# Kernel tuning notes

Hardware: AMD Instinct MI355X
Metric: run time of the kernel (lower is better)

The kernel has to match this reference:

```python
import jax, jax.numpy as jnp
import numpy as np

B, N, O, K, F = 4, 256, 5, 5, 256
H, D, DFF = 4, 64, 1024  # num_heads, KQ_len, FFN hidden
EPS = 1e-5


def setup_inputs() -> dict:
    key = jax.random.key(0)
    ks = jax.random.split(key, 16)
    s = 0.05
    p = lambda k, shape: (jax.random.normal(k, shape, jnp.float32) * s)
    return {
        "x": jax.random.normal(ks[0], (B, N, O, K, K, F), jnp.float32),
        "Wq": p(ks[1], (H * D, F)), "bq": p(ks[2], (H * D,)),
        "Wk": p(ks[3], (H * D, F)), "bk": p(ks[4], (H * D,)),
        "Wv": p(ks[5], (H * D, F)), "bv": p(ks[6], (H * D,)),
        "Wf": p(ks[7], (F, F)), "bf": p(ks[8], (F,)),
        "ln1_w": jnp.ones((N, O, F), jnp.float32), "ln1_b": jnp.zeros((N, O, F), jnp.float32),
        "ln2_w": jnp.ones((N, O, F), jnp.float32), "ln2_b": jnp.zeros((N, O, F), jnp.float32),
        "W1": p(ks[9], (DFF, F)), "b1": p(ks[10], (DFF,)),
        "W2": p(ks[11], (F, DFF)), "b2": p(ks[12], (F,)),
    }


def _layer_norm3(x, w, b):
    # torch LayerNorm with normalized_shape=[N, O, F]: stats over last 3 dims
    mu = jnp.mean(x, axis=(1, 2, 3), keepdims=True)
    var = jnp.var(x, axis=(1, 2, 3), keepdims=True)
    return (x - mu) * jax.lax.rsqrt(var + EPS) * w + b


def _split_heads(y):
    # [B,N,O,K,K,H*D] -> [B,N,O,H,K,K,D]
    return y.reshape(B, N, O, K, K, H, D).transpose(0, 1, 2, 5, 3, 4, 6)


def reference(x, Wq, bq, Wk, bk, Wv, bv, Wf, bf,
              ln1_w, ln1_b, ln2_w, ln2_b, W1, b1, W2, b2):
    q = _split_heads(x @ Wq.T + bq)
    k = _split_heads(x @ Wk.T + bk)
    v = _split_heads(x @ Wv.T + bv)
    c = K // 2
    qc = q[:, :, :, :, c, c, :]  # center query [B,N,O,H,D]
    # tile+mul+sum == dot of center query against every patch key
    scores = jnp.einsum('bnohd,bnohijd->bnohij', qc, k) / np.sqrt(float(D))
    w = jax.nn.softmax(scores.reshape(B, N, O, H, K * K), axis=-1)
    merged = jnp.einsum('bnohp,bnohpd->bnohd', w, v.reshape(B, N, O, H, K * K, D))
    merged = merged.reshape(B, N, O, H * D)
    attent = merged @ Wf.T + bf  # dropout = identity (eval)
    out1 = _layer_norm3(attent, ln1_w, ln1_b)
    ffn = jax.nn.relu(out1 @ W1.T + b1) @ W2.T + b2
    return _layer_norm3(out1 + ffn, ln2_w, ln2_b)
```

## Files before the change

kernel.cpp:

```cpp
#include <hip/hip_runtime.h>
#include <hip/hip_bf16.h>

#define FF 256
#define HH 4
#define DD 64
#define PP 25
#define SITES 5120
#define SPB 1280
#define DFF 1024
#define LN_ELEMS 327680

typedef const __hip_bfloat16* bfp;
typedef __hip_bfloat16* bfw;
typedef __attribute__((ext_vector_type(8))) short bf16x8;
typedef __attribute__((ext_vector_type(4))) float f32x4;

__device__ __forceinline__ float b2f(const __hip_bfloat16 v) { return __bfloat162float(v); }
__device__ __forceinline__ bool detect_bf(const unsigned* dt) {
    return dt[0] == 0x3F803F80u;
}
__device__ __forceinline__ float ldin(const void* p, size_t i, bool bf) {
    return bf ? __bfloat162float(((const __hip_bfloat16*)p)[i]) : ((const float*)p)[i];
}
__device__ __forceinline__ unsigned short f2bu(float f) {
    __hip_bfloat16 h = __float2bfloat16(f);
    return *(unsigned short*)&h;
}
__device__ __forceinline__ uint4 ldin8(const void* p, size_t i, bool bf) {
    if (bf) return *(const uint4*)((const unsigned short*)p + i);
    const float* f = (const float*)p + i;
    const float4 a = *(const float4*)f;
    const float4 b = *(const float4*)(f + 4);
    unsigned short u[8] = { f2bu(a.x), f2bu(a.y), f2bu(a.z), f2bu(a.w),
                            f2bu(b.x), f2bu(b.y), f2bu(b.z), f2bu(b.w) };
    return *(uint4*)u;
}

template<int RELU, int RES, int GATHER, int STATS, int BINT>
__global__ __launch_bounds__(256) void gemm_mfma(
    const void* xg, bfp Ab, int lda,
    const void* Bm, int ldb, const void* bias,
    bfp resid, int ldr, bfw C, int ldc, int Kc,
    int aoh, size_t boh, int bioh, int coh,
    float* __restrict__ red, const unsigned* dt)
{
    const bool bf = detect_bf(dt);
    const int h = blockIdx.z;
    Ab += (size_t)h * aoh;
    const size_t boff = (size_t)h * boh;
    const size_t biasoff = (size_t)h * bioh;
    C += (size_t)h * coh;

    __shared__ unsigned short Als[64][72];
    __shared__ unsigned short Bls[64][72];
    __shared__ float rs4[4], rss4[4];
    const int tid = threadIdx.x;
    const int lane = tid & 63;
    const int w = tid >> 6;
    const int m0 = blockIdx.y * 64;
    const int n0 = blockIdx.x * 64;
    const int r8 = tid >> 3;
    const int c8 = (tid & 7) * 8;

    f32x4 acc[4];
    #pragma unroll
    for (int mi = 0; mi < 4; ++mi) acc[mi] = (f32x4){0.f, 0.f, 0.f, 0.f};

    for (int k0 = 0; k0 < Kc; k0 += 64) {
        #pragma unroll
        for (int rr = 0; rr < 2; ++rr) {
            const int row = r8 + rr * 32;
            uint4 v;
            if (GATHER) v = ldin8(xg, ((size_t)(m0 + row) * PP + 12) * FF + (k0 + c8), bf);
            else        v = *(const uint4*)(Ab + (size_t)(m0 + row) * lda + (k0 + c8));
            *(uint4*)&Als[row][c8] = v;
        }
        #pragma unroll
        for (int rr = 0; rr < 2; ++rr) {
            const int row = r8 + rr * 32;
            const size_t bi = boff + (size_t)(n0 + row) * ldb + (k0 + c8);
            uint4 v;
            if (BINT) v = *(const uint4*)((const unsigned short*)Bm + bi);
            else      v = ldin8(Bm, bi, bf);
            *(uint4*)&Bls[row][c8] = v;
        }
        __syncthreads();
        #pragma unroll
        for (int ks = 0; ks < 2; ++ks) {
            const int kq = ks * 32 + (lane >> 4) * 8;
            const bf16x8 bfr = *(const bf16x8*)&Bls[w * 16 + (lane & 15)][kq];
            #pragma unroll
            for (int mi = 0; mi < 4; ++mi) {
                const bf16x8 afr = *(const bf16x8*)&Als[mi * 16 + (lane & 15)][kq];
                acc[mi] = __builtin_amdgcn_mfma_f32_16x16x32_bf16(afr, bfr, acc[mi], 0, 0, 0);
            }
        }
        __syncthreads();
    }

    const int col = n0 + w * 16 + (lane & 15);
    const int quad = lane >> 4;
    const float bvv = bias ? ldin(bias, biasoff + col, bf) : 0.f;
    float s_ = 0.f, ss_ = 0.f;
    #pragma unroll
    for (int mi = 0; mi < 4; ++mi) {
        #pragma unroll
        for (int r = 0; r < 4; ++r) {
            const int row = m0 + mi * 16 + quad * 4 + r;
            float v = acc[mi][r] + bvv;
            if (RES)  v += b2f(resid[(size_t)row * ldr + col]);
            if (RELU) v = fmaxf(v, 0.0f);
            if (STATS) { s_ += v; ss_ += v * v; }
            C[(size_t)row * ldc + col] = __float2bfloat16(v);
        }
    }
    if (STATS) {
        #pragma unroll
        for (int o = 32; o > 0; o >>= 1) { s_ += __shfl_down(s_, o); ss_ += __shfl_down(ss_, o); }
        if (lane == 0) { rs4[w] = s_; rss4[w] = ss_; }
        __syncthreads();
        if (tid == 0) {
            const int batch = m0 / SPB;
            atomicAdd(&red[batch * 2 + 0], rs4[0] + rs4[1] + rs4[2] + rs4[3]);
            atomicAdd(&red[batch * 2 + 1], rss4[0] + rss4[1] + rss4[2] + rss4[3]);
        }
    }
}

__global__ __launch_bounds__(256) void wkT_k(const void* Wk, bfw WkT, const unsigned* dt)
{
    const bool bf = detect_bf(dt);
    const int idx = blockIdx.x * 256 + threadIdx.x;
    const int d = idx & 63;
    const int f = (idx >> 6) & 255;
    const int h = idx >> 14;
    WkT[idx] = __float2bfloat16(ldin(Wk, (size_t)(h * DD + d) * FF + f, bf));
}

__global__ __launch_bounds__(256) void attn_site(const void* x, bfp qk, bfw xw,
                                                 const unsigned* dt)
{
    __shared__ unsigned short xsb[32][264];
    __shared__ unsigned short qkb[HH][FF];
    __shared__ float sc[HH][32];
    __shared__ float wl[HH][PP];

    const bool bf = detect_bf(dt);
    const int s = blockIdx.x;
    const int t = threadIdx.x;

    const size_t xbase = (size_t)s * (PP * FF);
    for (int e0 = t * 8; e0 < PP * FF; e0 += 2048)
        *(uint4*)&xsb[e0 >> 8][e0 & 255] = ldin8(x, xbase + e0, bf);
    if (t < 128)
        ((uint4*)qkb)[t] = ((const uint4*)(qk + (size_t)s * (HH * FF)))[t];
    __syncthreads();

    if (t < 64) {
        const int lane = t;
        const int col = lane & 15;
        const int quad = lane >> 4;
        const int brow = col & 3;
        f32x4 a0v = (f32x4){0.f, 0.f, 0.f, 0.f};
        f32x4 a1v = (f32x4){0.f, 0.f, 0.f, 0.f};
        #pragma unroll
        for (int ks = 0; ks < 8; ++ks) {
            const int kq = ks * 32 + quad * 8;
            const bf16x8 bfr = *(const bf16x8*)&qkb[brow][kq];
            const bf16x8 af0 = *(const bf16x8*)&xsb[col][kq];
            const bf16x8 af1 = *(const bf16x8*)&xsb[16 + col][kq];
            a0v = __builtin_amdgcn_mfma_f32_16x16x32_bf16(af0, bfr, a0v, 0, 0, 0);
            a1v = __builtin_amdgcn_mfma_f32_16x16x32_bf16(af1, bfr, a1v, 0, 0, 0);
        }
        if (col < HH) {
            #pragma unroll
            for (int r = 0; r < 4; ++r) {
                const int p = quad * 4 + r;
                sc[col][p] = a0v[r] * 0.125f;
                const int p2 = 16 + p;
                if (p2 < PP) sc[col][p2] = a1v[r] * 0.125f;
            }
        }
    }
    __syncthreads();

    if (t < HH) {
        float m = -1e30f;
        #pragma unroll
        for (int p = 0; p < PP; ++p) m = fmaxf(m, sc[t][p]);
        float e[PP], ssum = 0.f;
        #pragma unroll
        for (int p = 0; p < PP; ++p) { e[p] = __expf(sc[t][p] - m); ssum += e[p]; }
        const float inv = 1.f / ssum;
        #pragma unroll
        for (int p = 0; p < PP; ++p) wl[t][p] = e[p] * inv;
    }
    __syncthreads();

    float a0 = 0.f, a1 = 0.f, a2 = 0.f, a3 = 0.f;
    #pragma unroll
    for (int p = 0; p < PP; ++p) {
        const float xv = __bfloat162float(*(const __hip_bfloat16*)&xsb[p][t]);
        a0 = fmaf(wl[0][p], xv, a0);
        a1 = fmaf(wl[1][p], xv, a1);
        a2 = fmaf(wl[2][p], xv, a2);
        a3 = fmaf(wl[3][p], xv, a3);
    }
    bfw xwp = xw + (size_t)s * (HH * FF) + t;
    xwp[0 * FF] = __float2bfloat16(a0);
    xwp[1 * FF] = __float2bfloat16(a1);
    xwp[2 * FF] = __float2bfloat16(a2);
    xwp[3 * FF] = __float2bfloat16(a3);
}

template<int FINAL>
__global__ __launch_bounds__(256) void ln_apply(bfp X, const float* __restrict__ red,
                                                const void* w, const void* b,
                                                void* out, const unsigned* dt)
{
    const bool bf = detect_bf(dt);
    const int i8 = (blockIdx.x * 256 + threadIdx.x) * 8;
    const int s = i8 >> 8;
    const int batch = s / SPB;
    const int r = s - batch * SPB;
    const int f = i8 & 255;
    const float inv = 1.f / (float)LN_ELEMS;
    const float mu = red[batch * 2] * inv;
    const float var = red[batch * 2 + 1] * inv - mu * mu;
    const float rs = rsqrtf(var + 1e-5f);

    const uint4 xv = *(const uint4*)(X + i8);
    const uint4 wv = ldin8(w, (size_t)r * FF + f, bf);
    const uint4 bv = ldin8(b, (size_t)r * FF + f, bf);
    const unsigned short* xu = (const unsigned short*)&xv;
    const unsigned short* wu = (const unsigned short*)&wv;
    const unsigned short* bu = (const unsigned short*)&bv;
    float vo[8];
    #pragma unroll
    for (int j = 0; j < 8; ++j) {
        const float xf = __bfloat162float(*(const __hip_bfloat16*)&xu[j]);
        const float wf = __bfloat162float(*(const __hip_bfloat16*)&wu[j]);
        const float bf2 = __bfloat162float(*(const __hip_bfloat16*)&bu[j]);
        vo[j] = (xf - mu) * rs * wf + bf2;
    }
    if (FINAL && !bf) {
        float* o = (float*)out + i8;
        *(float4*)o = (float4){vo[0], vo[1], vo[2], vo[3]};
        *(float4*)(o + 4) = (float4){vo[4], vo[5], vo[6], vo[7]};
    } else {
        unsigned short ou[8];
        #pragma unroll
        for (int j = 0; j < 8; ++j) ou[j] = f2bu(vo[j]);
        *(uint4*)((unsigned short*)out + i8) = *(uint4*)ou;
    }
}

extern "C" void kernel_launch(void* const* d_in, const int* in_sizes, int n_in,
                              void* d_out, int out_size, void* d_ws, size_t ws_size,
                              hipStream_t stream)
{
    const void* x    = d_in[0];
    const void* Wq   = d_in[1];
    const void* bq   = d_in[2];
    const void* Wk   = d_in[3];
    const void* Wv   = d_in[5];
    const void* bv   = d_in[6];
    const void* Wf   = d_in[7];
    const void* bfv  = d_in[8];
    const void* ln1w = d_in[9];
    const void* ln1b = d_in[10];
    const void* ln2w = d_in[11];
    const void* ln2b = d_in[12];
    const void* W1   = d_in[13];
    const void* b1   = d_in[14];
    const void* W2   = d_in[15];
    const void* b2   = d_in[16];
    const unsigned* dt = (const unsigned*)d_in[9];

    char* w8 = (char*)d_ws;
    bfw qk   = (bfw)(w8);
    bfw xw   = (bfw)(w8 + 10485760);
    bfw hid  = (bfw)(w8 + 20971520);
    bfw WkT  = (bfw)(w8 + 31457280);
    bfw qc   = (bfw)(w8 + 32505856);
    bfw att  = (bfw)(w8 + 35127296);
    bfw out1 = (bfw)(w8 + 37748736);
    bfw z    = (bfw)(w8 + 40370176);
    float* red = (float*)(w8 + 42991616);

    hipMemsetAsync(red, 0, 64, stream);

    wkT_k<<<1024, 256, 0, stream>>>(Wk, WkT, dt);

    gemm_mfma<0, 0, 1, 0, 0><<<dim3(4, 80), 256, 0, stream>>>(
        x, nullptr, 0, Wq, FF, bq, nullptr, 0, qc, FF, FF, 0, 0, 0, 0, nullptr, dt);

    gemm_mfma<0, 0, 0, 0, 1><<<dim3(4, 80, HH), 256, 0, stream>>>(
        nullptr, qc, FF, WkT, DD, nullptr, nullptr, 0, qk, HH * FF, DD,
        DD, (size_t)FF * DD, 0, FF, nullptr, dt);

    attn_site<<<SITES, 256, 0, stream>>>(x, qk, xw, dt);

    gemm_mfma<0, 0, 0, 0, 0><<<dim3(1, 80, HH), 256, 0, stream>>>(
        nullptr, xw, HH * FF, Wv, FF, bv, nullptr, 0, qc, FF, FF,
        FF, (size_t)DD * FF, DD, DD, nullptr, dt);

    gemm_mfma<0, 0, 0, 1, 0><<<dim3(4, 80), 256, 0, stream>>>(
        nullptr, qc, FF, Wf, FF, bfv, nullptr, 0, att, FF, FF,
        0, 0, 0, 0, red, dt);

    ln_apply<0><<<640, 256, 0, stream>>>(att, red, ln1w, ln1b, out1, dt);

    gemm_mfma<1, 0, 0, 0, 0><<<dim3(16, 80), 256, 0, stream>>>(
        nullptr, out1, FF, W1, FF, b1, nullptr, 0, hid, DFF, FF,
        0, 0, 0, 0, nullptr, dt);

    gemm_mfma<0, 1, 0, 1, 0><<<dim3(4, 80), 256, 0, stream>>>(
        nullptr, hid, DFF, W2, DFF, b2, out1, FF, z, FF, DFF,
        0, 0, 0, 0, red + 8, dt);

    ln_apply<1><<<640, 256, 0, stream>>>(z, red + 8, ln2w, ln2b, d_out, dt);
}
```

Measured before the change: 336.9 us.

## Fold projection weights into combined matrices and prefetch GEMM tiles into registers

Weight-only products are precomputed so the per-site work changes shape. Mt = Wk_h^T Wq_h per head lets qk come from one GEMM of the centre x against Mt, with a bias vector built from bq and Wk. The V projection and the output projection are merged into one matrix Bvf = Wf·Wv_h, with a combined bias cf. Together these cut the per-site GEMM chain from four launches to two, plus small weight-only GEMMs. The GEMM kernel also loads the next K tile into registers while the current tile is being computed, at the cost of more registers. The merged output GEMM now has K=1024 instead of 256, and the extra weight GEMMs add launches that run every call.

```diff
diff --git a/kernel.cpp b/kernel.cpp
--- a/kernel.cpp
+++ b/kernel.cpp
@@ -33,6 +33,20 @@
     const float4 b = *(const float4*)(f + 4);
     unsigned short u[8] = { f2bu(a.x), f2bu(a.y), f2bu(a.z), f2bu(a.w),
                             f2bu(b.x), f2bu(b.y), f2bu(b.z), f2bu(b.w) };
+    return *(uint4*)u;
+}
+__device__ __forceinline__ void ldraw8(const void* p, size_t i, bool bf, uint4& lo, uint4& hi) {
+    if (bf) { lo = *(const uint4*)((const unsigned short*)p + i); return; }
+    const float* f = (const float*)p + i;
+    lo = *(const uint4*)f;
+    hi = *(const uint4*)(f + 4);
+}
+__device__ __forceinline__ uint4 cvt8(bool bf, uint4 lo, uint4 hi) {
+    if (bf) return lo;
+    const float* a = (const float*)&lo;
+    const float* b = (const float*)&hi;
+    unsigned short u[8] = { f2bu(a[0]), f2bu(a[1]), f2bu(a[2]), f2bu(a[3]),
+                            f2bu(b[0]), f2bu(b[1]), f2bu(b[2]), f2bu(b[3]) };
     return *(uint4*)u;
 }
 
@@ -66,25 +80,32 @@
     #pragma unroll
     for (int mi = 0; mi < 4; ++mi) acc[mi] = (f32x4){0.f, 0.f, 0.f, 0.f};
 
+    uint4 aLo0, aHi0, aLo1, aHi1, bLo0, bHi0, bLo1, bHi1;
+    auto fetch = [&](int kk) {
+        if (GATHER) {
+            ldraw8(xg, ((size_t)(m0 + r8) * PP + 12) * FF + (kk + c8), bf, aLo0, aHi0);
+            ldraw8(xg, ((size_t)(m0 + r8 + 32) * PP + 12) * FF + (kk + c8), bf, aLo1, aHi1);
+        } else {
+            aLo0 = *(const uint4*)(Ab + (size_t)(m0 + r8) * lda + (kk + c8));
+            aLo1 = *(const uint4*)(Ab + (size_t)(m0 + r8 + 32) * lda + (kk + c8));
+        }
+        if (BINT) {
+            bLo0 = *(const uint4*)((const unsigned short*)Bm + boff + (size_t)(n0 + r8) * ldb + (kk + c8));
+            bLo1 = *(const uint4*)((const unsigned short*)Bm + boff + (size_t)(n0 + r8 + 32) * ldb + (kk + c8));
+        } else {
+            ldraw8(Bm, boff + (size_t)(n0 + r8) * ldb + (kk + c8), bf, bLo0, bHi0);
+            ldraw8(Bm, boff + (size_t)(n0 + r8 + 32) * ldb + (kk + c8), bf, bLo1, bHi1);
+        }
+    };
+    fetch(0);
+
     for (int k0 = 0; k0 < Kc; k0 += 64) {
-        #pragma unroll
-        for (int rr = 0; rr < 2; ++rr) {
-            const int row = r8 + rr * 32;
-            uint4 v;
-            if (GATHER) v = ldin8(xg, ((size_t)(m0 + row) * PP + 12) * FF + (k0 + c8), bf);
-            else        v = *(const uint4*)(Ab + (size_t)(m0 + row) * lda + (k0 + c8));
-            *(uint4*)&Als[row][c8] = v;
-        }
-        #pragma unroll
-        for (int rr = 0; rr < 2; ++rr) {
-            const int row = r8 + rr * 32;
-            const size_t bi = boff + (size_t)(n0 + row) * ldb + (k0 + c8);
-            uint4 v;
-            if (BINT) v = *(const uint4*)((const unsigned short*)Bm + bi);
-            else      v = ldin8(Bm, bi, bf);
-            *(uint4*)&Bls[row][c8] = v;
-        }
+        *(uint4*)&Als[r8][c8]      = GATHER ? cvt8(bf, aLo0, aHi0) : aLo0;
+        *(uint4*)&Als[r8 + 32][c8] = GATHER ? cvt8(bf, aLo1, aHi1) : aLo1;
+        *(uint4*)&Bls[r8][c8]      = BINT ? bLo0 : cvt8(bf, bLo0, bHi0);
+        *(uint4*)&Bls[r8 + 32][c8] = BINT ? bLo1 : cvt8(bf, bLo1, bHi1);
         __syncthreads();
+        if (k0 + 64 < Kc) fetch(k0 + 64);
         #pragma unroll
         for (int ks = 0; ks < 2; ++ks) {
             const int kq = ks * 32 + (lane >> 4) * 8;
@@ -100,7 +121,8 @@
 
     const int col = n0 + w * 16 + (lane & 15);
     const int quad = lane >> 4;
-    const float bvv = bias ? ldin(bias, biasoff + col, bf) : 0.f;
+    const float bvv = bias ? (BINT ? ((const float*)bias)[biasoff + col]
+                                   : ldin(bias, biasoff + col, bf)) : 0.f;
     float s_ = 0.f, ss_ = 0.f;
     #pragma unroll
     for (int mi = 0; mi < 4; ++mi) {
@@ -127,14 +149,38 @@
     }
 }
 
-__global__ __launch_bounds__(256) void wkT_k(const void* Wk, bfw WkT, const unsigned* dt)
+__global__ __launch_bounds__(256) void prep(
+    const void* Wq, const void* Wk, const void* Wv, const void* Wf,
+    const void* bq, const void* bv, const void* bfv,
+    bfw WqT, bfw WkT, bfw WvT, bfw WfB,
+    float* __restrict__ rh, float* __restrict__ cf, const unsigned* dt)
 {
     const bool bf = detect_bf(dt);
-    const int idx = blockIdx.x * 256 + threadIdx.x;
-    const int d = idx & 63;
-    const int f = (idx >> 6) & 255;
-    const int h = idx >> 14;
-    WkT[idx] = __float2bfloat16(ldin(Wk, (size_t)(h * DD + d) * FF + f, bf));
+    const int bid = blockIdx.x;
+    const int t = threadIdx.x;
+    if (bid < 1024) {
+        const int gid = bid * 256 + t;
+        const int sec = gid >> 16;
+        const int i = gid & 65535;
+        if (sec == 3) { WfB[i] = __float2bfloat16(ldin(Wf, i, bf)); return; }
+        const int d = i & 63, f = (i >> 6) & 255, h = i >> 14;
+        const void* W = sec == 0 ? Wq : sec == 1 ? Wk : Wv;
+        bfw WT = sec == 0 ? WqT : sec == 1 ? WkT : WvT;
+        WT[i] = __float2bfloat16(ldin(W, (size_t)(h * DD + d) * FF + f, bf));
+        return;
+    }
+    if (bid < 1028) {
+        const int h = bid - 1024;
+        float acc = 0.f;
+        for (int d = 0; d < DD; ++d)
+            acc += ldin(bq, h * DD + d, bf) * ldin(Wk, (size_t)(h * DD + d) * FF + t, bf);
+        rh[h * FF + t] = acc;
+        return;
+    }
+    float acc = ldin(bfv, t, bf);
+    for (int j = 0; j < FF; ++j)
+        acc += ldin(Wf, (size_t)t * FF + j, bf) * ldin(bv, j, bf);
+    cf[t] = acc;
 }
 
 __global__ __launch_bounds__(256) void attn_site(const void* x, bfp qk, bfw xw,
@@ -281,32 +327,40 @@
     bfw qk   = (bfw)(w8);
     bfw xw   = (bfw)(w8 + 10485760);
     bfw hid  = (bfw)(w8 + 20971520);
-    bfw WkT  = (bfw)(w8 + 31457280);
-    bfw qc   = (bfw)(w8 + 32505856);
-    bfw att  = (bfw)(w8 + 35127296);
-    bfw out1 = (bfw)(w8 + 37748736);
-    bfw z    = (bfw)(w8 + 40370176);
-    float* red = (float*)(w8 + 42991616);
+    bfw WqT  = (bfw)(w8 + 31457280);
+    bfw WkT  = (bfw)(w8 + 31588352);
+    bfw WvT  = (bfw)(w8 + 31719424);
+    bfw WfB  = (bfw)(w8 + 31850496);
+    bfw Mt   = (bfw)(w8 + 31981568);
+    bfw Bvf  = (bfw)(w8 + 32505856);
+    bfw att  = (bfw)(w8 + 33030144);
+    bfw out1 = (bfw)(w8 + 35651584);
+    bfw z    = (bfw)(w8 + 38273024);
+    float* rh  = (float*)(w8 + 40894464);
+    float* cf  = (float*)(w8 + 40898560);
+    float* red = (float*)(w8 + 40899584);
 
     hipMemsetAsync(red, 0, 64, stream);
 
-    wkT_k<<<1024, 256, 0, stream>>>(Wk, WkT, dt);
-
-    gemm_mfma<0, 0, 1, 0, 0><<<dim3(4, 80), 256, 0, stream>>>(
-        x, nullptr, 0, Wq, FF, bq, nullptr, 0, qc, FF, FF, 0, 0, 0, 0, nullptr, dt);
-
-    gemm_mfma<0, 0, 0, 0, 1><<<dim3(4, 80, HH), 256, 0, stream>>>(
-        nullptr, qc, FF, WkT, DD, nullptr, nullptr, 0, qk, HH * FF, DD,
+    prep<<<1029, 256, 0, stream>>>(Wq, Wk, Wv, Wf, bq, bv, bfv,
+                                   WqT, WkT, WvT, WfB, rh, cf, dt);
+
+    gemm_mfma<0, 0, 0, 0, 1><<<dim3(4, 4, HH), 256, 0, stream>>>(
+        nullptr, WkT, DD, WqT, DD, nullptr, nullptr, 0, Mt, FF, DD,
+        FF * DD, (size_t)FF * DD, 0, FF * FF, nullptr, dt);
+
+    gemm_mfma<0, 0, 0, 0, 1><<<dim3(4, 4, HH), 256, 0, stream>>>(
+        nullptr, WfB, FF, WvT, DD, nullptr, nullptr, 0, Bvf, HH * FF, DD,
         DD, (size_t)FF * DD, 0, FF, nullptr, dt);
 
+    gemm_mfma<0, 0, 1, 0, 1><<<dim3(4, 80, HH), 256, 0, stream>>>(
+        x, nullptr, 0, Mt, FF, rh, nullptr, 0, qk, HH * FF, FF,
+        0, (size_t)FF * FF, FF, FF, nullptr, dt);
+
     attn_site<<<SITES, 256, 0, stream>>>(x, qk, xw, dt);
 
-    gemm_mfma<0, 0, 0, 0, 0><<<dim3(1, 80, HH), 256, 0, stream>>>(
-        nullptr, xw, HH * FF, Wv, FF, bv, nullptr, 0, qc, FF, FF,
-        FF, (size_t)DD * FF, DD, DD, nullptr, dt);
-
-    gemm_mfma<0, 0, 0, 1, 0><<<dim3(4, 80), 256, 0, stream>>>(
-        nullptr, qc, FF, Wf, FF, bfv, nullptr, 0, att, FF, FF,
+    gemm_mfma<0, 0, 0, 1, 1><<<dim3(4, 80), 256, 0, stream>>>(
+        nullptr, xw, HH * FF, Bvf, HH * FF, cf, nullptr, 0, att, FF, HH * FF,
         0, 0, 0, 0, red, dt);
 
     ln_apply<0><<<640, 256, 0, stream>>>(att, red, ln1w, ln1b, out1, dt);
```

Measured after the change: 350.6 us. +4.1%, slower.
